# Kernel tuning notes

Hardware: AMD Instinct MI355X
Metric: run time of the kernel (lower is better)

Reference implementation:

```python
import jax, jax.numpy as jnp
import numpy as np
import math

B, S, OBS, ACT = 64, 256, 96, 29
D, H, L, FF = 512, 8, 8, 2048
HD = D // H
EPS = 1e-5

def _ln(x, g, b):
    m = jnp.mean(x, axis=-1, keepdims=True)
    v = jnp.mean((x - m) ** 2, axis=-1, keepdims=True)
    return (x - m) * jax.lax.rsqrt(v + EPS) * g + b

def _pos_encoding():
    pos = jnp.arange(S, dtype=jnp.float32)[:, None]
    div = jnp.exp(jnp.arange(0, D, 2, dtype=jnp.float32) * (-math.log(10000.0) / D))
    pe = jnp.zeros((S, D), dtype=jnp.float32)
    pe = pe.at[:, 0::2].set(jnp.sin(pos * div))
    pe = pe.at[:, 1::2].set(jnp.cos(pos * div))
    return pe

def setup_inputs() -> dict:
    key = jax.random.key(0)
    ks = iter(jax.random.split(key, 64))
    def w(shape, scale=0.02):
        return jax.random.normal(next(ks), shape, dtype=jnp.float32) * scale
    inp = {
        "observations": jax.random.normal(next(ks), (B, S, OBS), dtype=jnp.float32),
        "W_in": w((OBS, D)), "b_in": jnp.zeros((D,)),
        "g_in": jnp.ones((D,)), "be_in": jnp.zeros((D,)),
        "Wq": w((L, D, D)), "bq": jnp.zeros((L, D)),
        "Wk": w((L, D, D)), "bk": jnp.zeros((L, D)),
        "Wv": w((L, D, D)), "bv": jnp.zeros((L, D)),
        "Wo": w((L, D, D)), "bo": jnp.zeros((L, D)),
        "g1": jnp.ones((L, D)), "be1": jnp.zeros((L, D)),
        "W1": w((L, D, FF)), "b1": jnp.zeros((L, FF)),
        "W2": w((L, FF, D)), "b2": jnp.zeros((L, D)),
        "g2": jnp.ones((L, D)), "be2": jnp.zeros((L, D)),
        "Wp1": w((D, D // 2)), "bp1": jnp.zeros((D // 2,)),
        "gp1": jnp.ones((D // 2,)), "bep1": jnp.zeros((D // 2,)),
        "Wp2": w((D // 2, D // 4)), "bp2": jnp.zeros((D // 4,)),
        "gp2": jnp.ones((D // 4,)), "bep2": jnp.zeros((D // 4,)),
        "Wp3": w((D // 4, ACT)), "bp3": jnp.zeros((ACT,)),
        "action_scale": jnp.ones((ACT,)), "action_bias": jnp.zeros((ACT,)),
    }
    return inp

def _forward(observations, W_in, b_in, g_in, be_in, Wq, bq, Wk, bk, Wv, bv, Wo, bo,
             g1, be1, W1, b1, W2, b2, g2, be2,
             Wp1, bp1, gp1, bep1, Wp2, bp2, gp2, bep2, Wp3, bp3,
             action_scale, action_bias):
    gelu = lambda x: jax.nn.gelu(x, approximate=False)
    # input projection + LN + GELU (dropout = identity in eval)
    x = gelu(_ln(observations @ W_in + b_in, g_in, be_in))
    x = x + _pos_encoding()[None, :, :]  # [B,S,D]
    scale = 1.0 / math.sqrt(HD)
    for l in range(L):
        q = (x @ Wq[l] + bq[l]).reshape(B, S, H, HD)
        k = (x @ Wk[l] + bk[l]).reshape(B, S, H, HD)
        v = (x @ Wv[l] + bv[l]).reshape(B, S, H, HD)
        scores = jnp.einsum('bqhd,bkhd->bhqk', q, k) * scale
        attn = jax.nn.softmax(scores, axis=-1)
        o = jnp.einsum('bhqk,bkhd->bqhd', attn, v).reshape(B, S, D)
        x = _ln(x + (o @ Wo[l] + bo[l]), g1[l], be1[l])
        h = gelu(x @ W1[l] + b1[l])
        x = _ln(x + (h @ W2[l] + b2[l]), g2[l], be2[l])
    y = gelu(_ln(x @ Wp1 + bp1, gp1, bep1))
    y = gelu(_ln(y @ Wp2 + bp2, gp2, bep2))
    actions = jnp.tanh(y @ Wp3 + bp3)
    return actions * action_scale + action_bias

def reference(observations, W_in, b_in, g_in, be_in, Wq, bq, Wk, bk, Wv, bv, Wo, bo,
              g1, be1, W1, b1, W2, b2, g2, be2,
              Wp1, bp1, gp1, bep1, Wp2, bp2, gp2, bep2, Wp3, bp3,
              action_scale, action_bias):
    return _forward(observations, W_in, b_in, g_in, be_in, Wq, bq, Wk, bk, Wv, bv, Wo, bo,
                    g1, be1, W1, b1, W2, b2, g2, be2,
                    Wp1, bp1, gp1, bep1, Wp2, bp2, gp2, bep2, Wp3, bp3,
                    action_scale, action_bias)
```

## Files before the change

kernel.cpp:

```cpp
#include <hip/hip_runtime.h>

typedef unsigned short u16;
typedef unsigned int u32;
typedef __attribute__((ext_vector_type(8))) __bf16 bf16x8;
typedef __attribute__((ext_vector_type(4))) float f32x4;
typedef __attribute__((ext_vector_type(2))) float f32x2;

#define B_ 64
#define S_ 256
#define OBS_ 96
#define ACT_ 29
#define D_ 512
#define H_ 8
#define L_ 8
#define FF_ 2048
#define HD_ 64
#define NTOK (B_ * S_)
#define QKV3 (3 * D_)

__device__ __forceinline__ u16 f2bf(float f) {
    __bf16 h = (__bf16)f;
    u16 u; __builtin_memcpy(&u, &h, 2); return u;
}
__device__ __forceinline__ float bf2f(u16 h) {
    return __uint_as_float(((u32)h) << 16);
}
__device__ __forceinline__ u16 f2h(float f) {
    _Float16 h = (_Float16)f;
    u16 u; __builtin_memcpy(&u, &h, 2); return u;
}
__device__ __forceinline__ float h2f(u16 u) {
    _Float16 h; __builtin_memcpy(&h, &u, 2); return (float)h;
}
__device__ __forceinline__ float gelu_f(float x) {
    const float k1 = 2.3022121f;
    const float k2 = 0.10294451f;
    float x2 = x * x;
    float arg = x * __builtin_fmaf(x2, k2, k1);
    float e = exp2f(arg);
    float r = __builtin_amdgcn_rcpf(1.0f + e);
    return __builtin_fmaf(-x, r, x);
}
__device__ __forceinline__ f32x2 gelu2(f32x2 x) {
    const float k1 = 2.3022121f;
    const float k2 = 0.10294451f;
    f32x2 x2 = x * x;
    f32x2 arg = x * (x2 * k2 + k1);
    f32x2 e;
    e.x = exp2f(arg.x);
    e.y = exp2f(arg.y);
    f32x2 one_e = e + 1.0f;
    f32x2 r;
    r.x = __builtin_amdgcn_rcpf(one_e.x);
    r.y = __builtin_amdgcn_rcpf(one_e.y);
    return x - x * r;
}
__device__ __forceinline__ void gld_lds16(const u16* g, u16* l) {
    __builtin_amdgcn_global_load_lds(
        (const __attribute__((address_space(1))) unsigned int*)g,
        (__attribute__((address_space(3))) unsigned int*)l, 16, 0, 0);
}

__global__ __launch_bounds__(256) void transpose_bf16_kernel(
    const float* __restrict__ src, u16* __restrict__ dst, int K, int N,
    size_t srcStride, size_t dstStride)
{
    __shared__ float tile[32][33];
    int n0 = blockIdx.x * 32, k0 = blockIdx.y * 32;
    const float* s = src + (size_t)blockIdx.z * srcStride;
    u16* d = dst + (size_t)blockIdx.z * dstStride;
    int tx = threadIdx.x, ty = threadIdx.y;
    for (int i = 0; i < 32; i += 8)
        tile[ty + i][tx] = s[(size_t)(k0 + ty + i) * N + n0 + tx];
    __syncthreads();
    for (int i = 0; i < 32; i += 8)
        d[(size_t)(n0 + ty + i) * K + k0 + tx] = f2bf(tile[tx][ty + i]);
}

__global__ __launch_bounds__(256) void concat_bias_kernel(
    const float* __restrict__ bq, const float* __restrict__ bk,
    const float* __restrict__ bv, float* __restrict__ dst)
{
    int i = blockIdx.x * 256 + threadIdx.x;
    int l = i / QKV3, r = i - l * QKV3;
    float v;
    if (r < D_)            v = bq[l * D_ + r];
    else if (r < 2 * D_)   v = bk[l * D_ + r - D_];
    else                   v = bv[l * D_ + r - 2 * D_];
    dst[i] = v;
}

__global__ __launch_bounds__(256) void in_gemm_kernel(
    const float* __restrict__ obs, const float* __restrict__ Win,
    const float* __restrict__ b_in, float* __restrict__ outp)
{
    __shared__ float As[OBS_][68];
    __shared__ float Bs[OBS_][68];
    int m0 = blockIdx.y * 64, n0 = blockIdx.x * 64;
    int t = threadIdx.x;
    #pragma unroll
    for (int i = 0; i < 24; i++) {
        int idx = i * 256 + t;
        int m = idx / OBS_, kk = idx - m * OBS_;
        As[kk][m] = obs[(size_t)(m0 + m) * OBS_ + kk];
    }
    #pragma unroll
    for (int i = 0; i < 24; i++) {
        int idx = i * 256 + t;
        int kk = idx >> 6, n = idx & 63;
        Bs[kk][n] = Win[(size_t)kk * D_ + n0 + n];
    }
    __syncthreads();
    int tm = t >> 4, tn = t & 15;
    float acc[4][4] = {};
    for (int kk = 0; kk < OBS_; kk++) {
        float4 a = *(const float4*)&As[kk][tm * 4];
        float4 b = *(const float4*)&Bs[kk][tn * 4];
        const float av[4] = {a.x, a.y, a.z, a.w};
        const float bv[4] = {b.x, b.y, b.z, b.w};
        #pragma unroll
        for (int r = 0; r < 4; r++)
            #pragma unroll
            for (int c = 0; c < 4; c++) acc[r][c] += av[r] * bv[c];
    }
    #pragma unroll
    for (int r = 0; r < 4; r++)
        #pragma unroll
        for (int c = 0; c < 4; c++) {
            int col = n0 + tn * 4 + c;
            outp[(size_t)(m0 + tm * 4 + r) * D_ + col] = acc[r][c] + b_in[col];
        }
}

template <int EPI, int TN, bool SPLITK>
__global__ __launch_bounds__(256, 3) void gemm_bt_kernel(
    const u16* __restrict__ A, const u16* __restrict__ BT,
    const float* __restrict__ bias, void* __restrict__ C,
    void* __restrict__ C2, int M, int N, int K, int kLen)
{
    constexpr int NI = TN / 32;
    constexpr int NB = TN / 32;
    __shared__ __align__(16) u16 smem[128 * 64 + TN * 64];
    u16* As = smem;
    u16* Bs = smem + 128 * 64;
    int bx = blockIdx.x;
    int m0 = (bx & 127) * 128, n0 = (bx >> 7) * TN;
    int z = SPLITK ? blockIdx.z : 0;
    int kStart = z * kLen;
    int t = threadIdx.x;
    int lane = t & 63, w = t >> 6;
    int wm = w >> 1, wn = w & 1;
    int l15 = lane & 15, quad = lane >> 4;

    int offC[4]; u16* lA[4];
    #pragma unroll
    for (int i = 0; i < 4; i++) {
        int ci = t + i * 256;
        int r = ci >> 3, s = ci & 7, gc = s ^ (r & 7);
        offC[i] = r * K + gc * 8;
        lA[i] = &As[ci * 8];
    }
    const u16* Abase = A + (size_t)m0 * K + kStart;
    const u16* Bbase = BT + (size_t)n0 * K + kStart;

    int aoff[2][4], boff[2][NI];
    #pragma unroll
    for (int kh = 0; kh < 2; kh++) {
        #pragma unroll
        for (int mi = 0; mi < 4; mi++) {
            int row = wm * 64 + mi * 16 + l15;
            aoff[kh][mi] = row * 64 + (((kh * 4 + quad) ^ (row & 7)) * 8);
        }
        #pragma unroll
        for (int ni = 0; ni < NI; ni++) {
            int row = wn * (TN / 2) + ni * 16 + l15;
            boff[kh][ni] = row * 64 + (((kh * 4 + quad) ^ (row & 7)) * 8);
        }
    }

    f32x4 acc[4][NI];
    f32x4 zero = {0.f, 0.f, 0.f, 0.f};
    #pragma unroll
    for (int mi = 0; mi < 4; mi++)
        #pragma unroll
        for (int ni = 0; ni < NI; ni++) acc[mi][ni] = zero;

    for (int kk = 0; kk < kLen; kk += 64) {
        __syncthreads();
        #pragma unroll
        for (int i = 0; i < 4; i++) gld_lds16(Abase + offC[i], lA[i]);
        #pragma unroll
        for (int i = 0; i < NB; i++) gld_lds16(Bbase + offC[i], lA[i] + 128 * 64);
        Abase += 64; Bbase += 64;
        __syncthreads();
        #pragma unroll
        for (int kh = 0; kh < 2; kh++) {
            bf16x8 a[4], b[NI];
            #pragma unroll
            for (int mi = 0; mi < 4; mi++)
                a[mi] = *(const bf16x8*)&As[aoff[kh][mi]];
            #pragma unroll
            for (int ni = 0; ni < NI; ni++)
                b[ni] = *(const bf16x8*)&Bs[boff[kh][ni]];
            #pragma unroll
            for (int mi = 0; mi < 4; mi++)
                #pragma unroll
                for (int ni = 0; ni < NI; ni++)
                    acc[mi][ni] = __builtin_amdgcn_mfma_f32_16x16x32_bf16(
                        a[mi], b[ni], acc[mi][ni], 0, 0, 0);
        }
    }

    bool partial = SPLITK && (z == 1);
    if (EPI == 2) {
        #pragma unroll
        for (int ni = 0; ni < NI; ni++) {
            int col = n0 + wn * (TN / 2) + ni * 16 + l15;
            float bv = partial ? 0.f : bias[col];
            #pragma unroll
            for (int mi = 0; mi < 4; mi++) {
                int rbase = m0 + wm * 64 + mi * 16 + quad * 4;
                f32x4 v = acc[mi][ni];
                #pragma unroll
                for (int r = 0; r < 4; r++)
                    ((float*)C)[(size_t)(rbase + r) * N + col] = v[r] + bv;
            }
        }
    } else {
        __syncthreads();
        u16* Ct = smem;
        #pragma unroll
        for (int ni = 0; ni < NI; ni++) {
            int colt = wn * (TN / 2) + ni * 16 + l15;
            float bv = partial ? 0.f : bias[n0 + colt];
            #pragma unroll
            for (int mi = 0; mi < 4; mi++) {
                int rbase = wm * 64 + mi * 16 + quad * 4;
                f32x4 v = acc[mi][ni];
                f32x2 y01 = {v[0], v[1]};
                f32x2 y23 = {v[2], v[3]};
                y01 = y01 + bv;
                y23 = y23 + bv;
                if (EPI == 1) { y01 = gelu2(y01); y23 = gelu2(y23); }
                const float ys[4] = {y01.x, y01.y, y23.x, y23.y};
                #pragma unroll
                for (int r = 0; r < 4; r++) {
                    u16 hv = (EPI == 3) ? f2h(ys[r]) : f2bf(ys[r]);
                    int row = rbase + r;
                    int cc = colt >> 3;
                    Ct[row * TN + (((cc ^ (row & 7)) * 8) | (colt & 7))] = hv;
                }
            }
        }
        __syncthreads();
        u16* dst = partial ? (u16*)C2 : (u16*)C;
        constexpr int CPR = TN / 8;
        #pragma unroll
        for (int i = 0; i < TN / 16; i++) {
            int ch = t + i * 256;
            int row = ch / CPR, cc = ch % CPR;
            uint4 vv = *(const uint4*)&Ct[row * TN + ((cc ^ (row & 7)) * 8)];
            *(uint4*)(dst + (size_t)(m0 + row) * N + n0 + cc * 8) = vv;
        }
    }
}

__global__ __launch_bounds__(256) void attn_kernel(
    const u16* __restrict__ qkv, u16* __restrict__ o)
{
    __shared__ __align__(16) u16 kvs[S_ * HD_];
    __shared__ __align__(16) u16 P[4 * 16 * S_];
    int bx = blockIdx.x;
    int qc = bx & 3;
    int h = (bx >> 2) & 7;
    int b = bx >> 5;
    int t = threadIdx.x;
    int lane = t & 63, w = t >> 6;
    int l15 = lane & 15, quad = lane >> 4;
    size_t rowb = (size_t)b * S_;

    {
        const u16* src = qkv + (rowb + t) * QKV3 + D_ + h * HD_;
        int sw = t & 7;
        #pragma unroll
        for (int j = 0; j < 8; j++)
            *(uint4*)&kvs[t * HD_ + ((j ^ sw) * 8)] = *(const uint4*)(src + j * 8);
    }
    bf16x8 aQ[2];
    {
        int qrow = qc * 64 + w * 16 + l15;
        const u16* src = qkv + (rowb + qrow) * QKV3 + h * HD_ + quad * 8;
        aQ[0] = *(const bf16x8*)(src);
        aQ[1] = *(const bf16x8*)(src + 32);
    }
    __syncthreads();

    f32x4 sc[16];
    #pragma unroll
    for (int nc = 0; nc < 16; nc++) {
        f32x4 acc = {0.f, 0.f, 0.f, 0.f};
        int row = nc * 16 + l15;
        int s0 = quad ^ (row & 7);
        bf16x8 b0 = *(const bf16x8*)&kvs[row * HD_ + s0 * 8];
        bf16x8 b1 = *(const bf16x8*)&kvs[row * HD_ + (s0 ^ 4) * 8];
        acc = __builtin_amdgcn_mfma_f32_16x16x32_bf16(aQ[0], b0, acc, 0, 0, 0);
        acc = __builtin_amdgcn_mfma_f32_16x16x32_bf16(aQ[1], b1, acc, 0, 0, 0);
        sc[nc] = acc;
    }
    const float scale = 0.125f;
    float rmax[4], rinv[4];
    #pragma unroll
    for (int r = 0; r < 4; r++) {
        float mx = -1e30f;
        #pragma unroll
        for (int nc = 0; nc < 16; nc++) mx = fmaxf(mx, sc[nc][r]);
        for (int off = 1; off < 16; off <<= 1) mx = fmaxf(mx, __shfl_xor(mx, off));
        rmax[r] = mx * scale;
    }
    #pragma unroll
    for (int r = 0; r < 4; r++) {
        float sum = 0.f;
        #pragma unroll
        for (int nc = 0; nc < 16; nc++) {
            float p = __expf(sc[nc][r] * scale - rmax[r]);
            sc[nc][r] = p;
            sum += p;
        }
        for (int off = 1; off < 16; off <<= 1) sum += __shfl_xor(sum, off);
        rinv[r] = 1.0f / sum;
    }
    #pragma unroll
    for (int nc = 0; nc < 16; nc++)
        #pragma unroll
        for (int r = 0; r < 4; r++) {
            int prow = quad * 4 + r;
            int col = nc * 16 + l15;
            int slot = (col >> 3) ^ (prow & 7);
            P[w * 4096 + prow * 256 + slot * 8 + (col & 7)] = f2bf(sc[nc][r]);
        }
    __syncthreads();

    {
        const u16* src = qkv + (rowb + t) * QKV3 + 2 * D_ + h * HD_;
        int chunkc = t >> 3, bytec = t & 7;
        #pragma unroll
        for (int dj = 0; dj < 8; dj++) {
            uint4 x = *(const uint4*)(src + dj * 8);
            const u16* xs = (const u16*)&x;
            #pragma unroll
            for (int i = 0; i < 8; i++) {
                int vrow = dj * 8 + i;
                kvs[vrow * 256 + ((chunkc ^ (vrow & 7)) * 8) + bytec] = xs[i];
            }
        }
    }
    __syncthreads();

    f32x4 accO[4];
    f32x4 zero = {0.f, 0.f, 0.f, 0.f};
    #pragma unroll
    for (int nt = 0; nt < 4; nt++) accO[nt] = zero;
    for (int ks = 0; ks < 8; ks++) {
        int ch = ks * 4 + quad;
        bf16x8 aP = *(const bf16x8*)&P[w * 4096 + l15 * 256 + ((ch ^ (l15 & 7)) * 8)];
        #pragma unroll
        for (int nt = 0; nt < 4; nt++) {
            int vrow = nt * 16 + l15;
            bf16x8 bV = *(const bf16x8*)&kvs[vrow * 256 + ((ch ^ (vrow & 7)) * 8)];
            accO[nt] = __builtin_amdgcn_mfma_f32_16x16x32_bf16(aP, bV, accO[nt], 0, 0, 0);
        }
    }
    __syncthreads();
    u16* Ot = P;
    #pragma unroll
    for (int nt = 0; nt < 4; nt++)
        #pragma unroll
        for (int r = 0; r < 4; r++) {
            int row = w * 16 + quad * 4 + r;
            int col = nt * 16 + l15;
            int cc = col >> 3;
            Ot[row * 64 + (((cc ^ (row & 7)) * 8) | (col & 7))] =
                f2bf(accO[nt][r] * rinv[r]);
        }
    __syncthreads();
    #pragma unroll
    for (int i = 0; i < 2; i++) {
        int ch = t + i * 256;
        int row = ch >> 3, cc = ch & 7;
        uint4 vv = *(const uint4*)&Ot[row * 64 + ((cc ^ (row & 7)) * 8)];
        *(uint4*)(o + (rowb + qc * 64 + row) * D_ + h * HD_ + cc * 8) = vv;
    }
}

template <int WIDTH, int INK, bool RES, bool GELU, bool PE, bool SUM2>
__global__ __launch_bounds__(256) void ln_kernel(
    const void* __restrict__ in, const void* __restrict__ in2,
    const u16* __restrict__ res,
    const float* __restrict__ g, const float* __restrict__ b,
    u16* __restrict__ out)
{
    constexpr int T = WIDTH / 4;
    constexpr int R = 256 / T;
    __shared__ float rs[R][2], rq[R][2];
    int t = threadIdx.x;
    int r = t / T, j = t % T;
    int row = blockIdx.x * R + r;
    size_t base = (size_t)row * WIDTH + j * 4;
    float v[4];
    if (INK == 0) {
        float4 x = *(const float4*)((const float*)in + base);
        v[0] = x.x; v[1] = x.y; v[2] = x.z; v[3] = x.w;
    } else {
        uint2 x = *(const uint2*)((const u16*)in + base);
        const u16* xs = (const u16*)&x;
        #pragma unroll
        for (int i = 0; i < 4; i++) v[i] = h2f(xs[i]);
    }
    if (SUM2) {
        if (INK == 0) {
            float4 x = *(const float4*)((const float*)in2 + base);
            v[0] += x.x; v[1] += x.y; v[2] += x.z; v[3] += x.w;
        } else {
            uint2 x = *(const uint2*)((const u16*)in2 + base);
            const u16* xs = (const u16*)&x;
            #pragma unroll
            for (int i = 0; i < 4; i++) v[i] += h2f(xs[i]);
        }
    }
    if (RES) {
        uint2 x = *(const uint2*)(res + base);
        const u16* xs = (const u16*)&x;
        #pragma unroll
        for (int i = 0; i < 4; i++) v[i] += bf2f(xs[i]);
    }
    float sm = v[0] + v[1] + v[2] + v[3];
    float sq = v[0] * v[0] + v[1] * v[1] + v[2] * v[2] + v[3] * v[3];
    if constexpr (T >= 64) {
        #pragma unroll
        for (int off = 32; off; off >>= 1) {
            sm += __shfl_xor(sm, off);
            sq += __shfl_xor(sq, off);
        }
    } else {
        #pragma unroll
        for (int off = 16; off; off >>= 1) {
            sm += __shfl_xor(sm, off, 32);
            sq += __shfl_xor(sq, off, 32);
        }
    }
    if constexpr (T == 128) {
        if ((t & 63) == 0) { rs[r][(t >> 6) & 1] = sm; rq[r][(t >> 6) & 1] = sq; }
        __syncthreads();
        sm = rs[r][0] + rs[r][1];
        sq = rq[r][0] + rq[r][1];
    }
    float mean = sm / (float)WIDTH;
    float var = sq / (float)WIDTH - mean * mean;
    float rstd = rsqrtf(var + 1e-5f);
    float4 gv = *(const float4*)(g + j * 4);
    float4 bv = *(const float4*)(b + j * 4);
    const float gs[4] = {gv.x, gv.y, gv.z, gv.w};
    const float bs[4] = {bv.x, bv.y, bv.z, bv.w};
    u16 o4[4];
    #pragma unroll
    for (int i = 0; i < 4; i++) {
        float y = (v[i] - mean) * rstd * gs[i] + bs[i];
        if (GELU) y = gelu_f(y);
        if (PE) {
            const float c = -9.210340371976184f / (float)D_;
            int s = row & (S_ - 1);
            int col = j * 4 + i;
            int i2 = col >> 1;
            float ang = (float)s * __expf((float)(2 * i2) * c);
            y += (col & 1) ? __cosf(ang) : __sinf(ang);
        }
        o4[i] = f2bf(y);
    }
    uint2 ov;
    ov.x = (u32)o4[0] | ((u32)o4[1] << 16);
    ov.y = (u32)o4[2] | ((u32)o4[3] << 16);
    *(uint2*)(out + base) = ov;
}

__global__ __launch_bounds__(256) void head_kernel(
    const u16* __restrict__ y2, const float* __restrict__ W,
    const float* __restrict__ bias, const float* __restrict__ scl,
    const float* __restrict__ bs, float* __restrict__ out)
{
    __shared__ float Ws[128 * ACT_];
    __shared__ u16 Ys[8 * 128];
    int t = threadIdx.x;
    for (int i = t; i < 128 * ACT_; i += 256) Ws[i] = W[i];
    int r0 = blockIdx.x * 8;
    for (int i = t; i < 8 * 128; i += 256) Ys[i] = y2[(size_t)r0 * 128 + i];
    __syncthreads();
    int lr = t >> 5, c = t & 31;
    if (c < ACT_) {
        float acc = bias[c];
        for (int kk = 0; kk < 128; kk++)
            acc += bf2f(Ys[lr * 128 + kk]) * Ws[kk * ACT_ + c];
        float y = tanhf(acc);
        out[(size_t)(r0 + lr) * ACT_ + c] = y * scl[c] + bs[c];
    }
}

extern "C" void kernel_launch(void* const* d_in, const int* in_sizes, int n_in,
                              void* d_out, int out_size, void* d_ws, size_t ws_size,
                              hipStream_t stream)
{
    const float* obs   = (const float*)d_in[0];
    const float* W_in  = (const float*)d_in[1];
    const float* b_in  = (const float*)d_in[2];
    const float* g_in  = (const float*)d_in[3];
    const float* be_in = (const float*)d_in[4];
    const float* Wq  = (const float*)d_in[5];
    const float* bq  = (const float*)d_in[6];
    const float* Wk  = (const float*)d_in[7];
    const float* bk  = (const float*)d_in[8];
    const float* Wv  = (const float*)d_in[9];
    const float* bv  = (const float*)d_in[10];
    const float* Wo  = (const float*)d_in[11];
    const float* bo  = (const float*)d_in[12];
    const float* g1  = (const float*)d_in[13];
    const float* be1 = (const float*)d_in[14];
    const float* W1  = (const float*)d_in[15];
    const float* b1  = (const float*)d_in[16];
    const float* W2  = (const float*)d_in[17];
    const float* b2  = (const float*)d_in[18];
    const float* g2  = (const float*)d_in[19];
    const float* be2 = (const float*)d_in[20];
    const float* Wp1  = (const float*)d_in[21];
    const float* bp1  = (const float*)d_in[22];
    const float* gp1  = (const float*)d_in[23];
    const float* bep1 = (const float*)d_in[24];
    const float* Wp2  = (const float*)d_in[25];
    const float* bp2  = (const float*)d_in[26];
    const float* gp2  = (const float*)d_in[27];
    const float* bep2 = (const float*)d_in[28];
    const float* Wp3  = (const float*)d_in[29];
    const float* bp3  = (const float*)d_in[30];
    const float* ascl = (const float*)d_in[31];
    const float* abias = (const float*)d_in[32];

    char* ws = (char*)d_ws;
    size_t off = 0;
    auto alloc = [&](size_t bytes) {
        void* p = ws + off;
        off += (bytes + 255) & ~(size_t)255;
        return p;
    };
    u16* WQKVT = (u16*)alloc((size_t)L_ * QKV3 * D_ * 2);
    u16* WOT   = (u16*)alloc((size_t)L_ * D_ * D_ * 2);
    u16* W1T   = (u16*)alloc((size_t)L_ * D_ * FF_ * 2);
    u16* W2T   = (u16*)alloc((size_t)L_ * FF_ * D_ * 2);
    u16* WP1T  = (u16*)alloc((size_t)D_ * (D_ / 2) * 2);
    u16* WP2T  = (u16*)alloc((size_t)(D_ / 2) * (D_ / 4) * 2);
    float* bqkv = (float*)alloc((size_t)L_ * QKV3 * 4);
    u16* x_bf = (u16*)alloc((size_t)NTOK * D_ * 2);
    float* tmp = (float*)alloc((size_t)NTOK * D_ * 4);
    char* regionA = (char*)alloc((size_t)NTOK * FF_ * 2);
    size_t base_need = off;
    char* tmp2 = ws + base_need;
    bool split = (ws_size >= base_need + (size_t)NTOK * D_ * 2);
    (void)in_sizes; (void)n_in; (void)out_size;

    u16* qkvbuf = (u16*)(regionA);
    u16* obuf = (u16*)(regionA + (size_t)NTOK * QKV3 * 2);
    u16* hbuf = (u16*)(regionA);
    u16* y1_bf = (u16*)(regionA);
    u16* y2_bf = (u16*)(regionA + (32u << 20));

    dim3 tb(32, 8);
    size_t DD = (size_t)D_ * D_;
    transpose_bf16_kernel<<<dim3(16, 16, L_), tb, 0, stream>>>(
        Wq, WQKVT, D_, D_, DD, (size_t)QKV3 * D_);
    transpose_bf16_kernel<<<dim3(16, 16, L_), tb, 0, stream>>>(
        Wk, WQKVT + DD, D_, D_, DD, (size_t)QKV3 * D_);
    transpose_bf16_kernel<<<dim3(16, 16, L_), tb, 0, stream>>>(
        Wv, WQKVT + 2 * DD, D_, D_, DD, (size_t)QKV3 * D_);
    transpose_bf16_kernel<<<dim3(16, 16, L_), tb, 0, stream>>>(
        Wo, WOT, D_, D_, DD, DD);
    transpose_bf16_kernel<<<dim3(64, 16, L_), tb, 0, stream>>>(
        W1, W1T, D_, FF_, (size_t)D_ * FF_, (size_t)D_ * FF_);
    transpose_bf16_kernel<<<dim3(16, 64, L_), tb, 0, stream>>>(
        W2, W2T, FF_, D_, (size_t)D_ * FF_, (size_t)D_ * FF_);
    transpose_bf16_kernel<<<dim3(8, 16, 1), tb, 0, stream>>>(
        Wp1, WP1T, D_, D_ / 2, 0, 0);
    transpose_bf16_kernel<<<dim3(4, 8, 1), tb, 0, stream>>>(
        Wp2, WP2T, D_ / 2, D_ / 4, 0, 0);
    concat_bias_kernel<<<L_ * QKV3 / 256, 256, 0, stream>>>(bq, bk, bv, bqkv);

    in_gemm_kernel<<<dim3(D_ / 64, NTOK / 64), 256, 0, stream>>>(
        obs, W_in, b_in, tmp);
    ln_kernel<D_, 0, false, true, true, false><<<NTOK / 2, 256, 0, stream>>>(
        tmp, nullptr, nullptr, g_in, be_in, x_bf);

    const int MG = NTOK / 128;
    for (int l = 0; l < L_; l++) {
        const u16* wqkvt = WQKVT + (size_t)l * QKV3 * D_;
        const u16* wot = WOT + (size_t)l * DD;
        const u16* w1t = W1T + (size_t)l * D_ * FF_;
        const u16* w2t = W2T + (size_t)l * FF_ * D_;

        gemm_bt_kernel<0, 128, false><<<MG * (QKV3 / 128), 256, 0, stream>>>(
            x_bf, wqkvt, bqkv + l * QKV3, qkvbuf, nullptr, NTOK, QKV3, D_, D_);
        attn_kernel<<<B_ * H_ * (S_ / 64), 256, 0, stream>>>(qkvbuf, obuf);
        if (split) {
            gemm_bt_kernel<3, 128, true><<<dim3(MG * 4, 1, 2), 256, 0, stream>>>(
                obuf, wot, bo + l * D_, tmp, tmp2, NTOK, D_, D_, D_ / 2);
            ln_kernel<D_, 1, true, false, false, true><<<NTOK / 2, 256, 0, stream>>>(
                tmp, tmp2, x_bf, g1 + l * D_, be1 + l * D_, x_bf);
        } else {
            gemm_bt_kernel<2, 128, false><<<MG * 4, 256, 0, stream>>>(
                obuf, wot, bo + l * D_, tmp, nullptr, NTOK, D_, D_, D_);
            ln_kernel<D_, 0, true, false, false, false><<<NTOK / 2, 256, 0, stream>>>(
                tmp, nullptr, x_bf, g1 + l * D_, be1 + l * D_, x_bf);
        }
        gemm_bt_kernel<1, 128, false><<<MG * (FF_ / 128), 256, 0, stream>>>(
            x_bf, w1t, b1 + l * FF_, hbuf, nullptr, NTOK, FF_, D_, D_);
        if (split) {
            gemm_bt_kernel<3, 128, true><<<dim3(MG * 4, 1, 2), 256, 0, stream>>>(
                hbuf, w2t, b2 + l * D_, tmp, tmp2, NTOK, D_, FF_, FF_ / 2);
            ln_kernel<D_, 1, true, false, false, true><<<NTOK / 2, 256, 0, stream>>>(
                tmp, tmp2, x_bf, g2 + l * D_, be2 + l * D_, x_bf);
        } else {
            gemm_bt_kernel<2, 128, false><<<MG * 4, 256, 0, stream>>>(
                hbuf, w2t, b2 + l * D_, tmp, nullptr, NTOK, D_, FF_, FF_);
            ln_kernel<D_, 0, true, false, false, false><<<NTOK / 2, 256, 0, stream>>>(
                tmp, nullptr, x_bf, g2 + l * D_, be2 + l * D_, x_bf);
        }
    }

    if (split) {
        gemm_bt_kernel<3, 64, true><<<dim3(MG * 4, 1, 2), 256, 0, stream>>>(
            x_bf, WP1T, bp1, tmp, tmp2, NTOK, D_ / 2, D_, D_ / 2);
        ln_kernel<D_ / 2, 1, false, true, false, true><<<NTOK / 4, 256, 0, stream>>>(
            tmp, tmp2, nullptr, gp1, bep1, y1_bf);
        gemm_bt_kernel<3, 64, true><<<dim3(MG * 2, 1, 2), 256, 0, stream>>>(
            y1_bf, WP2T, bp2, tmp, tmp2, NTOK, D_ / 4, D_ / 2, D_ / 4);
        ln_kernel<D_ / 4, 1, false, true, false, true><<<NTOK / 8, 256, 0, stream>>>(
            tmp, tmp2, nullptr, gp2, bep2, y2_bf);
    } else {
        gemm_bt_kernel<2, 64, false><<<MG * 4, 256, 0, stream>>>(
            x_bf, WP1T, bp1, tmp, nullptr, NTOK, D_ / 2, D_, D_);
        ln_kernel<D_ / 2, 0, false, true, false, false><<<NTOK / 4, 256, 0, stream>>>(
            tmp, nullptr, nullptr, gp1, bep1, y1_bf);
        gemm_bt_kernel<2, 64, false><<<MG * 2, 256, 0, stream>>>(
            y1_bf, WP2T, bp2, tmp, nullptr, NTOK, D_ / 4, D_ / 2, D_ / 2);
        ln_kernel<D_ / 4, 0, false, true, false, false><<<NTOK / 8, 256, 0, stream>>>(
            tmp, nullptr, nullptr, gp2, bep2, y2_bf);
    }
    head_kernel<<<NTOK / 8, 256, 0, stream>>>(
        y2_bf, Wp3, bp3, ascl, abias, (float*)d_out);
}
```

Measured before the change: 1.967 ms.

## Halve attention P shared buffer by staging scores in two passes; reorder block mapping

The attention kernel's probability tile in shared memory is halved (from 4x16x256 to 4x16x128 bf16). Probabilities are written and consumed in two halves, with extra barriers between them. This cuts LDS per block from 64KB to 48KB, which could let more blocks fit per CU. It also changes the blockIdx mapping so consecutive blocks share a batch's q-chunk across heads, which may improve L2 locality. The cost is two more __syncthreads and serialized P staging.

```diff
diff --git a/kernel.cpp b/kernel.cpp
--- a/kernel.cpp
+++ b/kernel.cpp
@@ -269,11 +269,11 @@
     const u16* __restrict__ qkv, u16* __restrict__ o)
 {
     __shared__ __align__(16) u16 kvs[S_ * HD_];
-    __shared__ __align__(16) u16 P[4 * 16 * S_];
-    int bx = blockIdx.x;
-    int qc = bx & 3;
-    int h = (bx >> 2) & 7;
-    int b = bx >> 5;
+    __shared__ __align__(16) u16 P[4 * 16 * 128];
+    int g = blockIdx.x;
+    int h = g & 7;
+    int qc = (g >> 3) & 3;
+    int b = g >> 5;
     int t = threadIdx.x;
     int lane = t & 63, w = t >> 6;
     int l15 = lane & 15, quad = lane >> 4;
@@ -330,13 +330,13 @@
         rinv[r] = 1.0f / sum;
     }
     #pragma unroll
-    for (int nc = 0; nc < 16; nc++)
+    for (int nc = 0; nc < 8; nc++)
         #pragma unroll
         for (int r = 0; r < 4; r++) {
             int prow = quad * 4 + r;
             int col = nc * 16 + l15;
             int slot = (col >> 3) ^ (prow & 7);
-            P[w * 4096 + prow * 256 + slot * 8 + (col & 7)] = f2bf(sc[nc][r]);
+            P[w * 2048 + prow * 128 + slot * 8 + (col & 7)] = f2bf(sc[nc][r]);
         }
     __syncthreads();
 
@@ -360,9 +360,33 @@
     f32x4 zero = {0.f, 0.f, 0.f, 0.f};
     #pragma unroll
     for (int nt = 0; nt < 4; nt++) accO[nt] = zero;
-    for (int ks = 0; ks < 8; ks++) {
+    for (int ks = 0; ks < 4; ks++) {
         int ch = ks * 4 + quad;
-        bf16x8 aP = *(const bf16x8*)&P[w * 4096 + l15 * 256 + ((ch ^ (l15 & 7)) * 8)];
+        bf16x8 aP = *(const bf16x8*)&P[w * 2048 + l15 * 128 + ((ch ^ (l15 & 7)) * 8)];
+        #pragma unroll
+        for (int nt = 0; nt < 4; nt++) {
+            int vrow = nt * 16 + l15;
+            bf16x8 bV = *(const bf16x8*)&kvs[vrow * 256 + ((ch ^ (vrow & 7)) * 8)];
+            accO[nt] = __builtin_amdgcn_mfma_f32_16x16x32_bf16(aP, bV, accO[nt], 0, 0, 0);
+        }
+    }
+    __syncthreads();
+
+    #pragma unroll
+    for (int nc = 8; nc < 16; nc++)
+        #pragma unroll
+        for (int r = 0; r < 4; r++) {
+            int prow = quad * 4 + r;
+            int col = (nc - 8) * 16 + l15;
+            int slot = (col >> 3) ^ (prow & 7);
+            P[w * 2048 + prow * 128 + slot * 8 + (col & 7)] = f2bf(sc[nc][r]);
+        }
+    __syncthreads();
+
+    for (int ks = 4; ks < 8; ks++) {
+        int ch = ks * 4 + quad;
+        int pc = ch - 16;
+        bf16x8 aP = *(const bf16x8*)&P[w * 2048 + l15 * 128 + ((pc ^ (l15 & 7)) * 8)];
         #pragma unroll
         for (int nt = 0; nt < 4; nt++) {
             int vrow = nt * 16 + l15;
```

After: 2.031 ms. 1.03x slower.
